# Performance work log

Hardware: AMD Instinct MI355X
Metric: run time of the kernel (lower is better)

The kernel has to match this reference:

```python
import jax, jax.numpy as jnp
import numpy as np

B, L, D, H, FF = 2, 2048, 2048, 16, 8192
DH = D // H
NEG = -1e9


def setup_inputs() -> dict:
    key = jax.random.key(0)
    ks = jax.random.split(key, 9)
    x = jax.random.normal(ks[0], (B, L, D), dtype=jnp.float32)
    # additive causal mask, broadcastable to [B, H, L, L]
    causal = jnp.triu(jnp.full((L, L), NEG, dtype=jnp.float32), k=1)
    mask = causal[None, None, :, :]
    s = 1.0 / np.sqrt(D)
    Wq = jax.random.normal(ks[1], (D, D), dtype=jnp.float32) * s
    Wk = jax.random.normal(ks[2], (D, D), dtype=jnp.float32) * s
    Wv = jax.random.normal(ks[3], (D, D), dtype=jnp.float32) * s
    Wo = jax.random.normal(ks[4], (D, D), dtype=jnp.float32) * s
    W_up = jax.random.normal(ks[5], (FF, D), dtype=jnp.float32) * s
    b_up = jnp.zeros((FF,), dtype=jnp.float32)
    W_down = jax.random.normal(ks[6], (D, FF), dtype=jnp.float32) * (1.0 / np.sqrt(FF))
    return {"x": x, "mask": mask, "Wq": Wq, "Wk": Wk, "Wv": Wv, "Wo": Wo,
            "W_up": W_up, "b_up": b_up, "W_down": W_down}


def reference(x, mask, Wq, Wk, Wv, Wo, W_up, b_up, W_down):
    b, l, d = x.shape
    # projections (torch Linear: y = x @ W.T); reshape to [B, H, L, DH]
    q = (x @ Wq.T).reshape(b, l, H, DH).transpose(0, 2, 1, 3)
    k = (x @ Wk.T).reshape(b, l, H, DH).transpose(0, 2, 1, 3)
    v = (x @ Wv.T).reshape(b, l, H, DH).transpose(0, 2, 1, 3)
    # NOTE: original module applies NO 1/sqrt(d_head) scaling
    scores = jnp.einsum('bhqd,bhkd->bhqk', q, k) + mask
    attn = jax.nn.softmax(scores, axis=-1)
    out = jnp.einsum('bhqk,bhkd->bhqd', attn, v)
    out = out.transpose(0, 2, 1, 3).reshape(b, l, d)
    x = x + out @ Wo.T
    h = jax.nn.relu(x @ W_up.T + b_up)
    return x + h @ W_down.T
```

## Files before the change

### kernel.cpp

```cpp
#include <hip/hip_runtime.h>
#include <stdint.h>

typedef _Float16 f16;
typedef __attribute__((ext_vector_type(8))) _Float16 f16x8;
typedef __attribute__((ext_vector_type(4))) _Float16 f16x4;
typedef __attribute__((ext_vector_type(2))) __fp16 fp16x2;
typedef __attribute__((ext_vector_type(4))) float f32x4;
typedef __attribute__((ext_vector_type(16))) float f32x16;
typedef __attribute__((ext_vector_type(4))) unsigned u32x4;

__device__ __forceinline__ void gload16(void* lds, const void* gc) {
  void* g = const_cast<void*>(gc);
  __builtin_amdgcn_global_load_lds((__attribute__((address_space(1))) void*)g,
                                   (__attribute__((address_space(3))) void*)lds,
                                   16, 0, 0);
}

__device__ __forceinline__ unsigned pkrtz(float a, float b) {
  union { fp16x2 h; unsigned u; } c;
  c.h = __builtin_amdgcn_cvt_pkrtz(a, b);
  return c.u;
}

__global__ __launch_bounds__(256) void k_cast(const float* __restrict__ in,
                                              f16* __restrict__ out, int n4) {
  int stride = gridDim.x * blockDim.x;
  for (int i = blockIdx.x * blockDim.x + threadIdx.x; i < n4; i += stride) {
    float4 v = ((const float4*)in)[i];
    f16x4 o;
    o[0] = (f16)v.x; o[1] = (f16)v.y; o[2] = (f16)v.z; o[3] = (f16)v.w;
    ((f16x4*)out)[i] = o;
  }
}

__global__ __launch_bounds__(256) void k_cast4(const float* __restrict__ s0, const float* __restrict__ s1,
                                               const float* __restrict__ s2, const float* __restrict__ s3,
                                               f16* __restrict__ d0, f16* __restrict__ d1,
                                               f16* __restrict__ d2, f16* __restrict__ d3, int n4) {
  const int which = blockIdx.y;
  const float* in = which == 0 ? s0 : which == 1 ? s1 : which == 2 ? s2 : s3;
  f16* out = which == 0 ? d0 : which == 1 ? d1 : which == 2 ? d2 : d3;
  int stride = gridDim.x * blockDim.x;
  for (int i = blockIdx.x * blockDim.x + threadIdx.x; i < n4; i += stride) {
    float4 v = ((const float4*)in)[i];
    f16x4 o;
    o[0] = (f16)v.x; o[1] = (f16)v.y; o[2] = (f16)v.z; o[3] = (f16)v.w;
    ((f16x4*)out)[i] = o;
  }
}

__global__ __launch_bounds__(256) void k_cast2w(const float* __restrict__ s0, const float* __restrict__ s1,
                                                f16* __restrict__ d0, f16* __restrict__ d1, int n4) {
  const int which = blockIdx.y;
  const float* in = which == 0 ? s0 : s1;
  f16* out = which == 0 ? d0 : d1;
  int stride = gridDim.x * blockDim.x;
  for (int i = blockIdx.x * blockDim.x + threadIdx.x; i < n4; i += stride) {
    float4 v = ((const float4*)in)[i];
    f16x4 o;
    o[0] = (f16)v.x; o[1] = (f16)v.y; o[2] = (f16)v.z; o[3] = (f16)v.w;
    ((f16x4*)out)[i] = o;
  }
}

__global__ __launch_bounds__(256) void k_transpose_v(const f16* __restrict__ vp,
                                                     f16* __restrict__ vt) {
  __shared__ __attribute__((aligned(16))) f16 tile[64][66];
  const int lt = blockIdx.x, dt = blockIdx.y, bh = blockIdx.z;
  const int t = threadIdx.x;
  const int r = t >> 3, c = 8 * (t & 7);
  const f16* src = vp + ((size_t)bh * 2048 + lt * 64) * 128 + dt * 64;
#pragma unroll
  for (int i = 0; i < 2; ++i) {
    union { f16x8 v; unsigned u[4]; } uu;
    uu.v = *(const f16x8*)&src[(size_t)(i * 32 + r) * 128 + c];
#pragma unroll
    for (int j = 0; j < 4; ++j)
      *(unsigned*)&tile[i * 32 + r][c + 2 * j] = uu.u[j];
  }
  __syncthreads();
  f16* dst = vt + ((size_t)bh * 128 + dt * 64) * 2048 + lt * 64;
#pragma unroll
  for (int i = 0; i < 2; ++i) {
    const int dr = i * 32 + r;
    f16x8 o;
#pragma unroll
    for (int e = 0; e < 8; ++e) o[e] = tile[c + e][dr];
    *(f16x8*)&dst[(size_t)dr * 2048 + c] = o;
  }
}

__global__ __launch_bounds__(256) void k_fuseout(const f16* __restrict__ x1b,
                                                 const float* __restrict__ p0,
                                                 const float* __restrict__ p1,
                                                 float* __restrict__ out, int n4) {
  int stride = gridDim.x * blockDim.x;
  for (int i = blockIdx.x * blockDim.x + threadIdx.x; i < n4; i += stride) {
    float4 a = ((const float4*)p0)[i];
    float4 b = ((const float4*)p1)[i];
    f16x4 xb = ((const f16x4*)x1b)[i];
    float4 o;
    o.x = (float)xb[0] + a.x + b.x;
    o.y = (float)xb[1] + a.y + b.y;
    o.z = (float)xb[2] + a.z + b.z;
    o.w = (float)xb[3] + a.w + b.w;
    ((float4*)out)[i] = o;
  }
}

template <int EPI, int SPLITOUT, int BK>
__global__ __launch_bounds__(256, 4) void gemm_nt(const f16* __restrict__ A,
                                                  const f16* __restrict__ B,
                                                  int Kit, int ld, int N,
                                                  const float* __restrict__ res,
                                                  f16* __restrict__ outb) {
  constexpr int TSZ = 128 * BK;
  constexpr int CH  = 2048;
  constexpr int RPC = CH / BK;
  constexpr int NCH = 128 / RPC;
  constexpr int CW  = BK / 8;
  __shared__ __attribute__((aligned(16))) f16 As[TSZ];
  __shared__ __attribute__((aligned(16))) f16 Bs[TSZ];
  const int t = threadIdx.x;
  const int l = t & 63;
  const int w = t >> 6;
  const int wr = w >> 1, wc = w & 1;

  const int nwg = gridDim.x * gridDim.y;
  const int id = blockIdx.y * gridDim.x + blockIdx.x;
  const int sw = (id & 7) * (nwg >> 3) + (id >> 3);
  const int bn = sw % gridDim.x;
  const int bm = sw / gridDim.x;

  f32x4 acc[4][4] = {};

  const size_t aoff = (size_t)bm * 128 * ld;
  const size_t boff = (size_t)bn * 128 * ld;

  const int sr = t / CW;
  const int sc = 8 * (t % CW);
  const int lbase = w * 512;

  const int lr = l & 15, lq = l >> 4;
  const int nk = Kit / BK;
  for (int kt = 0; kt < nk; ++kt) {
    const size_t gbase = (size_t)kt * BK + (size_t)sr * ld + sc;
#pragma unroll
    for (int j = 0; j < NCH; ++j) {
      gload16(As + j * CH + lbase, A + aoff + (size_t)j * RPC * ld + gbase);
      gload16(Bs + j * CH + lbase, B + boff + (size_t)j * RPC * ld + gbase);
    }
    __syncthreads();
#pragma unroll
    for (int kk = 0; kk < BK / 32; ++kk) {
      f16x8 af[4], bfr[4];
#pragma unroll
      for (int m = 0; m < 4; ++m)
        af[m] = *(const f16x8*)&As[(wr * 64 + m * 16 + lr) * BK + kk * 32 + 8 * lq];
#pragma unroll
      for (int n = 0; n < 4; ++n)
        bfr[n] = *(const f16x8*)&Bs[(wc * 64 + n * 16 + lr) * BK + kk * 32 + 8 * lq];
#pragma unroll
      for (int m = 0; m < 4; ++m)
#pragma unroll
        for (int n = 0; n < 4; ++n)
          acc[m][n] = __builtin_amdgcn_mfma_f32_16x16x32_f16(af[m], bfr[n], acc[m][n], 0, 0, 0);
    }
    __syncthreads();
  }

#pragma unroll
  for (int m = 0; m < 4; ++m) {
#pragma unroll
    for (int r = 0; r < 4; ++r) {
      const int grow = bm * 128 + wr * 64 + m * 16 + lq * 4 + r;
#pragma unroll
      for (int n = 0; n < 4; ++n) {
        const int gcol = bn * 128 + wc * 64 + n * 16 + lr;
        const size_t idx = (size_t)grow * N + gcol;
        outb[idx] = (f16)(res[idx] + acc[m][n][r]);
      }
    }
  }
}

template <int EPI, int SPLITOUT>
__global__ __launch_bounds__(512, 2) void gemm8(const f16* __restrict__ A,
                                                const f16* __restrict__ B,
                                                int Kit, int ld, int N,
                                                const float* __restrict__ bias,
                                                float* __restrict__ outf,
                                                float* __restrict__ outf2,
                                                f16* __restrict__ outb,
                                                f16* __restrict__ outb_lo,
                                                f16* __restrict__ outv) {
  __shared__ __attribute__((aligned(16))) f16 As[2 * 16384];
  __shared__ __attribute__((aligned(16))) f16 Bs[2 * 16384];
  const int t = threadIdx.x;
  const int l = t & 63;
  const int w = t >> 6;
  const int wm = w >> 2, wn = w & 3;

  const int nwg = gridDim.x * gridDim.y;
  const int id = blockIdx.y * gridDim.x + blockIdx.x;
  const int sw = (id & 7) * (nwg >> 3) + (id >> 3);
  const int bn = sw % gridDim.x;
  const int bm = sw / gridDim.x;
  const int k0 = blockIdx.z * Kit;

  const size_t aoff = (size_t)(bm * 256) * ld + k0;
  const size_t boff = (size_t)(bn * 256) * ld + k0;

  const int rstage = t >> 3;
  const int gstage = (t & 7) ^ ((t >> 3) & 7);
  const int ldsb = (t >> 6) * 512;

  auto stage = [&](int tt, int b) {
    const size_t col = (size_t)tt * 64 + gstage * 8;
#pragma unroll
    for (int j = 0; j < 4; ++j) {
      const size_t grow = (size_t)(j * 64 + rstage) * ld + col;
      gload16(As + b * 16384 + j * 4096 + ldsb, A + aoff + grow);
      gload16(Bs + b * 16384 + j * 4096 + ldsb, B + boff + grow);
    }
  };

  f32x4 acc[8][4] = {};

  const int lr = l & 15, lq = l >> 4;
  const int x7 = lr & 7;
  const int nt = Kit >> 6;

  stage(0, 0);
  stage(1, 1);
  asm volatile("s_waitcnt vmcnt(8)" ::: "memory");
  __builtin_amdgcn_s_barrier();

  for (int kt = 0; kt < nt; ++kt) {
    const int b = kt & 1;
    const f16* Ab = As + b * 16384;
    const f16* Bb = Bs + b * 16384;
    f16x8 af[4][2], bf[4][2];
#pragma unroll
    for (int m = 0; m < 4; ++m)
#pragma unroll
      for (int ks = 0; ks < 2; ++ks)
        af[m][ks] = *(const f16x8*)&Ab[((wm * 128 + m * 16 + lr) * 8 + ((ks * 4 + lq) ^ x7)) * 8];
#pragma unroll
    for (int n = 0; n < 4; ++n)
#pragma unroll
      for (int ks = 0; ks < 2; ++ks)
        bf[n][ks] = *(const f16x8*)&Bb[((wn * 64 + n * 16 + lr) * 8 + ((ks * 4 + lq) ^ x7)) * 8];
    __builtin_amdgcn_s_barrier();
    __builtin_amdgcn_s_setprio(1);
#pragma unroll
    for (int m = 0; m < 4; ++m)
#pragma unroll
      for (int n = 0; n < 2; ++n)
#pragma unroll
        for (int ks = 0; ks < 2; ++ks)
          acc[m][n] = __builtin_amdgcn_mfma_f32_16x16x32_f16(af[m][ks], bf[n][ks], acc[m][n], 0, 0, 0);
    __builtin_amdgcn_s_setprio(0);
    __builtin_amdgcn_s_barrier();
    __builtin_amdgcn_s_setprio(1);
#pragma unroll
    for (int m = 0; m < 4; ++m)
#pragma unroll
      for (int n = 2; n < 4; ++n)
#pragma unroll
        for (int ks = 0; ks < 2; ++ks)
          acc[m][n] = __builtin_amdgcn_mfma_f32_16x16x32_f16(af[m][ks], bf[n][ks], acc[m][n], 0, 0, 0);
    __builtin_amdgcn_s_setprio(0);
    __builtin_amdgcn_s_barrier();
#pragma unroll
    for (int m = 0; m < 4; ++m)
#pragma unroll
      for (int ks = 0; ks < 2; ++ks)
        af[m][ks] = *(const f16x8*)&Ab[((wm * 128 + 64 + m * 16 + lr) * 8 + ((ks * 4 + lq) ^ x7)) * 8];
    asm volatile("s_waitcnt lgkmcnt(0)" ::: "memory");
    __builtin_amdgcn_sched_barrier(0);
    __builtin_amdgcn_s_barrier();
    if (kt + 2 < nt) stage(kt + 2, b);
    __builtin_amdgcn_s_setprio(1);
#pragma unroll
    for (int m = 0; m < 4; ++m)
#pragma unroll
      for (int n = 0; n < 2; ++n)
#pragma unroll
        for (int ks = 0; ks < 2; ++ks)
          acc[4 + m][n] = __builtin_amdgcn_mfma_f32_16x16x32_f16(af[m][ks], bf[n][ks], acc[4 + m][n], 0, 0, 0);
    __builtin_amdgcn_s_setprio(0);
    __builtin_amdgcn_s_barrier();
    __builtin_amdgcn_s_setprio(1);
#pragma unroll
    for (int m = 0; m < 4; ++m)
#pragma unroll
      for (int n = 2; n < 4; ++n)
#pragma unroll
        for (int ks = 0; ks < 2; ++ks)
          acc[4 + m][n] = __builtin_amdgcn_mfma_f32_16x16x32_f16(af[m][ks], bf[n][ks], acc[4 + m][n], 0, 0, 0);
    __builtin_amdgcn_s_setprio(0);
    if (kt + 2 < nt) {
      asm volatile("s_waitcnt vmcnt(8)" ::: "memory");
    } else {
      asm volatile("s_waitcnt vmcnt(0)" ::: "memory");
    }
    __builtin_amdgcn_s_barrier();
  }

  const size_t QKS = (size_t)8 << 20;
#pragma unroll
  for (int m = 0; m < 8; ++m) {
#pragma unroll
    for (int r = 0; r < 4; ++r) {
      const int grow = bm * 256 + wm * 128 + m * 16 + lq * 4 + r;
#pragma unroll
      for (int n = 0; n < 4; ++n) {
        const int gcol = bn * 256 + wn * 64 + n * 16 + lr;
        const float v = acc[m][n][r];
        if constexpr (EPI == 0) {
          const int which = gcol >> 11;
          const int hcol = gcol & 2047;
          const int bb = grow >> 11, ll = grow & 2047;
          const int hh = hcol >> 7, dh = hcol & 127;
          const size_t idx = ((size_t)((bb * 16 + hh) * 2048 + ll) << 7) + dh;
          const f16 hv = (f16)v;
          if (which == 2) {
            outv[idx] = hv;
          } else {
            outb[which * QKS + idx] = hv;
            if constexpr (SPLITOUT) outb_lo[which * QKS + idx] = (f16)(v - (float)hv);
          }
        } else if constexpr (EPI == 2) {
          const size_t idx = (size_t)grow * N + gcol;
          outb[idx] = (f16)fmaxf(v + bias[gcol], 0.f);
        } else {
          const size_t idx = (size_t)grow * N + gcol;
          (blockIdx.z ? outf2 : outf)[idx] = v;
        }
      }
    }
  }
}

__global__ __launch_bounds__(256) void k_attn(const f16* __restrict__ q_hi,
                                              const f16* __restrict__ q_lo,
                                              const f16* __restrict__ k_hi,
                                              const f16* __restrict__ k_lo,
                                              const f16* __restrict__ vtp,
                                              f16* __restrict__ op) {
  __shared__ __attribute__((aligned(16))) f16 Ks_hi[64 * 128];
  __shared__ __attribute__((aligned(16))) f16 Ks_lo[64 * 128];
  __shared__ __attribute__((aligned(16))) f16 Vs[128 * 64];
  const int t = threadIdx.x, l = t & 63, w = t >> 6;
  const int flat = (int)blockIdx.x;
  const int s_ = flat >> 5;
  const int bh = flat & 31;
  const int qb = (s_ < 8) ? (15 - s_) : (s_ - 8);
  const int q0 = qb * 128;
  const int lh = l >> 5, lm = l & 31;
  const int wrow0 = q0 + 32 * w;
  const int myrow = wrow0 + lm;

  const f16* qhp = q_hi + (size_t)bh * 2048 * 128;
  const f16* qlp = q_lo + (size_t)bh * 2048 * 128;
  const f16* khp = k_hi + (size_t)bh * 2048 * 128;
  const f16* klp = k_lo + (size_t)bh * 2048 * 128;
  const f16* vhp = vtp + (size_t)bh * 128 * 2048;

  const int krow = t >> 4, kg = t & 15;
  const int vrow = t >> 3, vg = t & 7;

  f16x8 aqh[8], aql[8];
#pragma unroll
  for (int c = 0; c < 8; ++c) {
    const size_t qi = (size_t)myrow * 128 + c * 16 + 8 * lh;
    aqh[c] = *(const f16x8*)&qhp[qi];
    aql[c] = *(const f16x8*)&qlp[qi];
  }

  f32x16 acc[4] = {};
  float mr = -1e30f, sr = 0.f;

  const int ntile = 2 * qb + 2;
  for (int kt = 0; kt < ntile; ++kt) {
    f16x8 tkh[4], tkl[4], tv[4];
#pragma unroll
    for (int i = 0; i < 4; ++i) {
      const size_t ki = (size_t)(kt * 64 + i * 16 + krow) * 128 + 8 * kg;
      tkh[i] = *(const f16x8*)&khp[ki];
      tkl[i] = *(const f16x8*)&klp[ki];
      tv[i] = *(const f16x8*)&vhp[(size_t)(i * 32 + vrow) * 2048 + kt * 64 + 8 * vg];
    }
    __syncthreads();
#pragma unroll
    for (int i = 0; i < 4; ++i) {
      const int kr = i * 16 + krow;
      const int g = kg ^ (kr & 7);
      *(f16x8*)&Ks_hi[kr * 128 + 8 * g] = tkh[i];
      *(f16x8*)&Ks_lo[kr * 128 + 8 * g] = tkl[i];
      const int vr = i * 32 + vrow;
      const int gv = vg ^ (vr & 7);
      *(f16x8*)&Vs[vr * 64 + 8 * gv] = tv[i];
    }
    __syncthreads();

    if (kt * 64 >= wrow0 + 32) continue;

    f32x16 s0, s1;
    __builtin_amdgcn_s_setprio(1);
    {
      f32x16 zh = {}, zl = {};
#pragma unroll
      for (int c = 0; c < 8; ++c) {
        const int g = (2 * c + lh) ^ (lm & 7);
        const f16x8 bh_ = *(const f16x8*)&Ks_hi[lm * 128 + 8 * g];
        const f16x8 bl_ = *(const f16x8*)&Ks_lo[lm * 128 + 8 * g];
        zh = __builtin_amdgcn_mfma_f32_32x32x16_f16(bh_, aqh[c], zh, 0, 0, 0);
        zl = __builtin_amdgcn_mfma_f32_32x32x16_f16(bh_, aql[c], zl, 0, 0, 0);
        zl = __builtin_amdgcn_mfma_f32_32x32x16_f16(bl_, aqh[c], zl, 0, 0, 0);
      }
      s0 = zh + zl;
    }
    {
      f32x16 zh = {}, zl = {};
#pragma unroll
      for (int c = 0; c < 8; ++c) {
        const int g = (2 * c + lh) ^ (lm & 7);
        const f16x8 bh_ = *(const f16x8*)&Ks_hi[(32 + lm) * 128 + 8 * g];
        const f16x8 bl_ = *(const f16x8*)&Ks_lo[(32 + lm) * 128 + 8 * g];
        zh = __builtin_amdgcn_mfma_f32_32x32x16_f16(bh_, aqh[c], zh, 0, 0, 0);
        zl = __builtin_amdgcn_mfma_f32_32x32x16_f16(bh_, aql[c], zl, 0, 0, 0);
        zl = __builtin_amdgcn_mfma_f32_32x32x16_f16(bl_, aqh[c], zl, 0, 0, 0);
      }
      s1 = zh + zl;
    }
    __builtin_amdgcn_s_setprio(0);

    if (kt * 64 + 63 > wrow0) {
#pragma unroll
      for (int j = 0; j < 16; ++j) {
        const int keyl = (j & 3) + 8 * (j >> 2) + 4 * lh;
        if (kt * 64 + keyl > myrow) s0[j] = -1e30f;
        if (kt * 64 + 32 + keyl > myrow) s1[j] = -1e30f;
      }
    }

    float m = -1e30f;
#pragma unroll
    for (int j = 0; j < 16; ++j) m = fmaxf(m, fmaxf(s0[j], s1[j]));
    m = fmaxf(m, __shfl_xor(m, 32));
    if (__any(m > mr + 8.f)) {
      const float mnew = fmaxf(mr, m);
      const float sc = __expf(mr - mnew);
      mr = mnew;
      sr *= sc;
#pragma unroll
      for (int j = 0; j < 16; ++j) {
        const float scj = __shfl(sc, (j & 3) + 8 * (j >> 2) + 4 * lh);
#pragma unroll
        for (int ct = 0; ct < 4; ++ct) acc[ct][j] *= scj;
      }
    }
    float p0v[16], p1v[16];
    float ts = 0.f;
#pragma unroll
    for (int j = 0; j < 16; ++j) {
      p0v[j] = __expf(s0[j] - mr);
      p1v[j] = __expf(s1[j] - mr);
      ts += p0v[j] + p1v[j];
    }
    sr += ts + __shfl_xor(ts, 32);

    unsigned u[16];
#pragma unroll
    for (int m2 = 0; m2 < 8; ++m2) {
      u[m2] = pkrtz(p0v[2 * m2], p0v[2 * m2 + 1]);
      u[8 + m2] = pkrtz(p1v[2 * m2], p1v[2 * m2 + 1]);
    }
    unsigned ys[8];
#pragma unroll
    for (int m2 = 0; m2 < 8; ++m2) {
      const int q_ = m2 >> 1, h_ = m2 & 1;
      const unsigned xs = lh ? u[4 * q_ + h_] : u[4 * q_ + 2 + h_];
      ys[m2] = __shfl_xor(xs, 32);
    }
    f16x8 pf[4];
#pragma unroll
    for (int kk = 0; kk < 4; ++kk) {
      union { u32x4 u4; f16x8 h8; } cv;
      if (lh == 0) {
        cv.u4[0] = u[4 * kk];     cv.u4[1] = u[4 * kk + 1];
        cv.u4[2] = ys[2 * kk];    cv.u4[3] = ys[2 * kk + 1];
      } else {
        cv.u4[0] = ys[2 * kk];    cv.u4[1] = ys[2 * kk + 1];
        cv.u4[2] = u[4 * kk + 2]; cv.u4[3] = u[4 * kk + 3];
      }
      pf[kk] = cv.h8;
    }

    __builtin_amdgcn_s_setprio(1);
#pragma unroll
    for (int ct = 0; ct < 4; ++ct) {
      const int dcol = ct * 32 + lm;
#pragma unroll
      for (int kk = 0; kk < 4; ++kk) {
        const int gv = (2 * kk + lh) ^ (dcol & 7);
        const f16x8 bv = *(const f16x8*)&Vs[dcol * 64 + 8 * gv];
        acc[ct] = __builtin_amdgcn_mfma_f32_32x32x16_f16(pf[kk], bv, acc[ct], 0, 0, 0);
      }
    }
    __builtin_amdgcn_s_setprio(0);
  }

  const int bb = bh >> 4, hh = bh & 15;
  const float inv = 1.f / sr;
#pragma unroll
  for (int j = 0; j < 16; ++j) {
    const int rl = (j & 3) + 8 * (j >> 2) + 4 * lh;
    const float invj = __shfl(inv, rl);
    const size_t row = (size_t)(bb * 2048 + wrow0 + rl);
#pragma unroll
    for (int ct = 0; ct < 4; ++ct)
      op[row * 2048 + hh * 128 + ct * 32 + lm] = (f16)(acc[ct][j] * invj);
  }
}

extern "C" void kernel_launch(void* const* d_in, const int* in_sizes, int n_in,
                              void* d_out, int out_size, void* d_ws, size_t ws_size,
                              hipStream_t stream) {
  const float* x   = (const float*)d_in[0];
  const float* Wq  = (const float*)d_in[2];
  const float* Wk  = (const float*)d_in[3];
  const float* Wv  = (const float*)d_in[4];
  const float* Wo  = (const float*)d_in[5];
  const float* Wup = (const float*)d_in[6];
  const float* bup = (const float*)d_in[7];
  const float* Wdn = (const float*)d_in[8];
  float* out = (float*)d_out;

  const size_t M1 = 1u << 20;
  f16* W = (f16*)d_ws;
  f16* x_hi    = W + 0 * M1;
  f16* wqkv_hi = W + 8 * M1;
  f16* wo_hi   = W + 20 * M1;
  f16* wup_hi  = W + 24 * M1;
  f16* wdn_hi  = W + 40 * M1;
  f16* q_hi    = W + 56 * M1;
  f16* q_lo    = W + 72 * M1;
  f16* vp      = W + 88 * M1;
  f16* vtb     = W + 96 * M1;
  f16* x1b   = x_hi;
  float* p0  = (float*)(W + 24 * M1);
  f16* hb    = W + 56 * M1;
  float* p1  = (float*)(W + 88 * M1);
  f16* attno = vp;
  if (ws_size < (size_t)104 * M1 * sizeof(f16)) return;

  auto cg = [](size_t n4) { size_t g = (n4 + 255) / 256; return (unsigned)(g > 2048 ? 2048 : g); };
  dim3 b256(256);
  dim3 b512(512);
  k_cast<<<cg(2 * M1), b256, 0, stream>>>(x, x_hi, (int)(2 * M1));
  k_cast4<<<dim3(cg(1 * M1), 4), b256, 0, stream>>>(
      Wq, Wk, Wv, Wo,
      wqkv_hi, wqkv_hi + 4 * M1, wqkv_hi + 8 * M1, wo_hi, (int)(1 * M1));
  k_cast2w<<<dim3(cg(4 * M1), 2), b256, 0, stream>>>(
      Wup, Wdn, wup_hi, wdn_hi, (int)(4 * M1));

  gemm8<0, 1><<<dim3(24, 16), b512, 0, stream>>>(
      x_hi, wqkv_hi, 2048, 2048, 6144,
      nullptr, nullptr, nullptr, q_hi, q_lo, vp);
  k_transpose_v<<<dim3(32, 2, 32), b256, 0, stream>>>(vp, vtb);
  k_attn<<<dim3(512), b256, 0, stream>>>(
      q_hi, q_lo, q_hi + 8 * M1, q_lo + 8 * M1, vtb, attno);
  gemm_nt<1, 0, 64><<<dim3(16, 32), b256, 0, stream>>>(
      attno, wo_hi, 2048, 2048, 2048, x, x1b);
  gemm8<2, 0><<<dim3(32, 16), b512, 0, stream>>>(
      x1b, wup_hi, 2048, 2048, 8192,
      bup, nullptr, nullptr, hb, nullptr, nullptr);
  gemm8<3, 0><<<dim3(8, 16, 2), b512, 0, stream>>>(
      hb, wdn_hi, 4096, 8192, 2048,
      nullptr, p0, p1, nullptr, nullptr, nullptr);
  k_fuseout<<<2048, b256, 0, stream>>>(x1b, p0, p1, out, (int)(2 * M1));
}
```

Before: 722.9 us.

## Restructure gemm8 main loop into 4-buffer K=32 pipeline with fewer barriers

The 256x256 GEMM main loop is reworked. K steps of 64 with double buffering become K steps of 32 in a 4-slot LDS ring, with three tiles in flight. The per-iteration body now loads all A/B fragments once and issues 32 MFMAs under a single barrier, replacing the interleaved half-tile phases with several barriers. The LDS swizzle is changed to suit 32-wide rows. This aims to cut barrier and synchronisation overhead and deepen memory prefetch, but shorter K steps give less MFMA work per barrier and lose the prior fine-grained compute/load interleaving.

```diff
diff --git a/kernel.cpp b/kernel.cpp
--- a/kernel.cpp
+++ b/kernel.cpp
@@ -194,8 +194,8 @@
                                                 f16* __restrict__ outb,
                                                 f16* __restrict__ outb_lo,
                                                 f16* __restrict__ outv) {
-  __shared__ __attribute__((aligned(16))) f16 As[2 * 16384];
-  __shared__ __attribute__((aligned(16))) f16 Bs[2 * 16384];
+  __shared__ __attribute__((aligned(16))) f16 As[4 * 8192];
+  __shared__ __attribute__((aligned(16))) f16 Bs[4 * 8192];
   const int t = threadIdx.x;
   const int l = t & 63;
   const int w = t >> 6;
@@ -211,97 +211,59 @@
   const size_t aoff = (size_t)(bm * 256) * ld + k0;
   const size_t boff = (size_t)(bn * 256) * ld + k0;
 
-  const int rstage = t >> 3;
-  const int gstage = (t & 7) ^ ((t >> 3) & 7);
+  const int r0 = t >> 2;
+  const int gsw = (t & 3) ^ (r0 & 3) ^ ((r0 >> 2) & 3);
   const int ldsb = (t >> 6) * 512;
 
   auto stage = [&](int tt, int b) {
-    const size_t col = (size_t)tt * 64 + gstage * 8;
-#pragma unroll
-    for (int j = 0; j < 4; ++j) {
-      const size_t grow = (size_t)(j * 64 + rstage) * ld + col;
-      gload16(As + b * 16384 + j * 4096 + ldsb, A + aoff + grow);
-      gload16(Bs + b * 16384 + j * 4096 + ldsb, B + boff + grow);
+    const size_t col = (size_t)tt * 32 + gsw * 8;
+#pragma unroll
+    for (int j = 0; j < 2; ++j) {
+      const size_t grow = (size_t)(j * 128 + r0) * ld + col;
+      gload16(As + b * 8192 + j * 4096 + ldsb, A + aoff + grow);
+      gload16(Bs + b * 8192 + j * 4096 + ldsb, B + boff + grow);
     }
   };
 
   f32x4 acc[8][4] = {};
 
   const int lr = l & 15, lq = l >> 4;
-  const int x7 = lr & 7;
-  const int nt = Kit >> 6;
+  const int xg = (lr & 3) ^ ((lr >> 2) & 3);
+  const int nt = Kit >> 5;
 
   stage(0, 0);
   stage(1, 1);
+  stage(2, 2);
   asm volatile("s_waitcnt vmcnt(8)" ::: "memory");
   __builtin_amdgcn_s_barrier();
 
   for (int kt = 0; kt < nt; ++kt) {
-    const int b = kt & 1;
-    const f16* Ab = As + b * 16384;
-    const f16* Bb = Bs + b * 16384;
-    f16x8 af[4][2], bf[4][2];
-#pragma unroll
-    for (int m = 0; m < 4; ++m)
-#pragma unroll
-      for (int ks = 0; ks < 2; ++ks)
-        af[m][ks] = *(const f16x8*)&Ab[((wm * 128 + m * 16 + lr) * 8 + ((ks * 4 + lq) ^ x7)) * 8];
-#pragma unroll
-    for (int n = 0; n < 4; ++n)
-#pragma unroll
-      for (int ks = 0; ks < 2; ++ks)
-        bf[n][ks] = *(const f16x8*)&Bb[((wn * 64 + n * 16 + lr) * 8 + ((ks * 4 + lq) ^ x7)) * 8];
-    __builtin_amdgcn_s_barrier();
+    const int b = kt & 3;
+    const f16* Ab = As + b * 8192;
+    const f16* Bb = Bs + b * 8192;
+    f16x8 af[8], bf[4];
+#pragma unroll
+    for (int m = 0; m < 8; ++m) {
+      const int row = wm * 128 + m * 16 + lr;
+      af[m] = *(const f16x8*)&Ab[row * 32 + (lq ^ xg) * 8];
+    }
+#pragma unroll
+    for (int n = 0; n < 4; ++n) {
+      const int row = wn * 64 + n * 16 + lr;
+      bf[n] = *(const f16x8*)&Bb[row * 32 + (lq ^ xg) * 8];
+    }
+    if (kt + 3 < nt) stage(kt + 3, (kt + 3) & 3);
     __builtin_amdgcn_s_setprio(1);
 #pragma unroll
-    for (int m = 0; m < 4; ++m)
-#pragma unroll
-      for (int n = 0; n < 2; ++n)
-#pragma unroll
-        for (int ks = 0; ks < 2; ++ks)
-          acc[m][n] = __builtin_amdgcn_mfma_f32_16x16x32_f16(af[m][ks], bf[n][ks], acc[m][n], 0, 0, 0);
+    for (int m = 0; m < 8; ++m)
+#pragma unroll
+      for (int n = 0; n < 4; ++n)
+        acc[m][n] = __builtin_amdgcn_mfma_f32_16x16x32_f16(af[m], bf[n], acc[m][n], 0, 0, 0);
     __builtin_amdgcn_s_setprio(0);
-    __builtin_amdgcn_s_barrier();
-    __builtin_amdgcn_s_setprio(1);
-#pragma unroll
-    for (int m = 0; m < 4; ++m)
-#pragma unroll
-      for (int n = 2; n < 4; ++n)
-#pragma unroll
-        for (int ks = 0; ks < 2; ++ks)
-          acc[m][n] = __builtin_amdgcn_mfma_f32_16x16x32_f16(af[m][ks], bf[n][ks], acc[m][n], 0, 0, 0);
-    __builtin_amdgcn_s_setprio(0);
-    __builtin_amdgcn_s_barrier();
-#pragma unroll
-    for (int m = 0; m < 4; ++m)
-#pragma unroll
-      for (int ks = 0; ks < 2; ++ks)
-        af[m][ks] = *(const f16x8*)&Ab[((wm * 128 + 64 + m * 16 + lr) * 8 + ((ks * 4 + lq) ^ x7)) * 8];
-    asm volatile("s_waitcnt lgkmcnt(0)" ::: "memory");
-    __builtin_amdgcn_sched_barrier(0);
-    __builtin_amdgcn_s_barrier();
-    if (kt + 2 < nt) stage(kt + 2, b);
-    __builtin_amdgcn_s_setprio(1);
-#pragma unroll
-    for (int m = 0; m < 4; ++m)
-#pragma unroll
-      for (int n = 0; n < 2; ++n)
-#pragma unroll
-        for (int ks = 0; ks < 2; ++ks)
-          acc[4 + m][n] = __builtin_amdgcn_mfma_f32_16x16x32_f16(af[m][ks], bf[n][ks], acc[4 + m][n], 0, 0, 0);
-    __builtin_amdgcn_s_setprio(0);
-    __builtin_amdgcn_s_barrier();
-    __builtin_amdgcn_s_setprio(1);
-#pragma unroll
-    for (int m = 0; m < 4; ++m)
-#pragma unroll
-      for (int n = 2; n < 4; ++n)
-#pragma unroll
-        for (int ks = 0; ks < 2; ++ks)
-          acc[4 + m][n] = __builtin_amdgcn_mfma_f32_16x16x32_f16(af[m][ks], bf[n][ks], acc[4 + m][n], 0, 0, 0);
-    __builtin_amdgcn_s_setprio(0);
-    if (kt + 2 < nt) {
+    if (kt + 3 < nt) {
       asm volatile("s_waitcnt vmcnt(8)" ::: "memory");
+    } else if (kt + 2 < nt) {
+      asm volatile("s_waitcnt vmcnt(4)" ::: "memory");
     } else {
       asm volatile("s_waitcnt vmcnt(0)" ::: "memory");
     }
```

Result: no change. 710.5 us (-1.7%).
